# Performance work log

Measured on AMD Instinct MI355X. Metric: run time of the kernel, lower is better.

## Reference

```python
import jax, jax.numpy as jnp
import numpy as np

N_VOX = 100000   # active voxels
K = 27           # 3^3 kernel offsets
M = 60000        # matched (in, out) pairs per offset
CIN = 64
COUT = 64
BN_EPS = 1e-5


def setup_inputs() -> dict:
    key = jax.random.key(0)
    ks = jax.random.split(key, 6)
    feats = jax.random.normal(ks[0], (N_VOX, CIN), dtype=jnp.float32)
    W = jax.random.normal(ks[1], (K, CIN, COUT), dtype=jnp.float32) * 0.05
    gamma = jnp.ones((COUT,), dtype=jnp.float32)
    beta = jnp.zeros((COUT,), dtype=jnp.float32)
    running_mean = jax.random.normal(ks[2], (COUT,), dtype=jnp.float32) * 0.1
    running_var = jax.random.uniform(ks[3], (COUT,), dtype=jnp.float32, minval=0.5, maxval=1.5)
    in_idx = jax.random.randint(ks[4], (K, M), 0, N_VOX, dtype=jnp.int32)
    out_idx = jax.random.randint(ks[5], (K, M), 0, N_VOX, dtype=jnp.int32)
    return {
        "feats": feats, "W": W, "gamma": gamma, "beta": beta,
        "running_mean": running_mean, "running_var": running_var,
        "in_idx": in_idx, "out_idx": out_idx,
    }


def reference(feats, W, gamma, beta, running_mean, running_var, in_idx, out_idx):
    # Sparse conv as gather-GEMM-scatter over the hash-map kernel map.
    gathered = feats[in_idx]                              # [K, M, Cin]
    contrib = jnp.einsum('kmc,kcd->kmd', gathered, W)     # [K, M, Cout]
    out = jax.ops.segment_sum(
        contrib.reshape(-1, W.shape[-1]),                 # [K*M, Cout]
        out_idx.reshape(-1),
        num_segments=feats.shape[0],
    )                                                     # [N, Cout]
    # BatchNorm (inference, running stats) + ReLU
    inv = jax.lax.rsqrt(running_var + BN_EPS)
    y = (out - running_mean) * (inv * gamma) + beta
    return jnp.maximum(y, 0.0)
```

## Files before the change

kernel.cpp:

```cpp
#include <hip/hip_runtime.h>

#define N_VOX 100000
#define K_OFF 27
#define M_PAIR 60000
#define NPAIR (K_OFF * M_PAIR)
#define CIN 64
#define COUT 64
#define BN_EPS 1e-5f

#define VB_SHIFT 8
#define VB (1 << VB_SHIFT)
#define NB ((N_VOX + VB - 1) / VB)
#define BCAP 5120
#define PPT 16
#define PA_PAIRS (256 * PPT)
#define PA_GRID ((NPAIR + PA_PAIRS - 1) / PA_PAIRS)

#define TILES_PER_WAVE 10
#define WAVES_PER_K (M_PAIR / 16 / TILES_PER_WAVE)
#define CONV_BLOCKS_X ((WAVES_PER_K + 3) / 4)

typedef __attribute__((ext_vector_type(8))) short bf16x8;
typedef __attribute__((ext_vector_type(8))) unsigned short u16x8;
typedef __attribute__((ext_vector_type(2))) unsigned int u32x2;
typedef __attribute__((ext_vector_type(4))) float f32x4;

__device__ __forceinline__ unsigned short f32_to_bf16(float f) {
    unsigned int u = __float_as_uint(f);
    u += 0x7FFFu + ((u >> 16) & 1u);
    return (unsigned short)(u >> 16);
}
__device__ __forceinline__ float bf16_lo(unsigned int u) {
    return __uint_as_float(u << 16);
}
__device__ __forceinline__ float bf16_hi(unsigned int u) {
    return __uint_as_float(u & 0xffff0000u);
}
__device__ __forceinline__ float bf16_to_f32(unsigned short b) {
    return __uint_as_float(((unsigned int)b) << 16);
}

__global__ __launch_bounds__(256) void scatter_pairs_kernel(
    const int* __restrict__ oix,
    unsigned int* __restrict__ recs, int* __restrict__ bucketCount,
    const float* __restrict__ feats, unsigned short* __restrict__ fb,
    const float* __restrict__ W, unsigned short* __restrict__ Wt,
    const float* __restrict__ gamma, const float* __restrict__ beta,
    const float* __restrict__ rmean, const float* __restrict__ rvar,
    float* __restrict__ bnscale, float* __restrict__ bnshift)
{
    __shared__ int lhist[NB];
    __shared__ int gbase[NB];
    const int t = threadIdx.x;
    for (int i = t; i < NB; i += 256) lhist[i] = 0;
    __syncthreads();

    const int base = blockIdx.x * PA_PAIRS;
    int vsave[PPT];
    int lpos[PPT];
#pragma unroll
    for (int i = 0; i < PPT; ++i) {
        const int e = base + i * 256 + t;
        int v = -1, lp = 0;
        if (e < NPAIR) {
            v = oix[e];
            lp = atomicAdd(&lhist[v >> VB_SHIFT], 1);
        }
        vsave[i] = v;
        lpos[i] = lp;
    }
    __syncthreads();
    for (int i = t; i < NB; i += 256) {
        const int c = lhist[i];
        gbase[i] = c ? atomicAdd(&bucketCount[i], c) : 0;
    }
    __syncthreads();
#pragma unroll
    for (int i = 0; i < PPT; ++i) {
        const int v = vsave[i];
        if (v >= 0) {
            const int e = base + i * 256 + t;
            const int b = v >> VB_SHIFT;
            const int idx = gbase[b] + lpos[i];
            if (idx < BCAP)
                recs[(size_t)b * BCAP + idx] =
                    ((unsigned int)e << VB_SHIFT) | (unsigned int)(v & (VB - 1));
        }
    }

    const int gid = blockIdx.x * 256 + t;
    const int nt = PA_GRID * 256;
    for (int e4i = gid; e4i < (N_VOX * CIN) / 4; e4i += nt) {
        const int e4 = e4i * 4;
        const float4 v = *(const float4*)(feats + e4);
        ushort4 b;
        b.x = f32_to_bf16(v.x);
        b.y = f32_to_bf16(v.y);
        b.z = f32_to_bf16(v.z);
        b.w = f32_to_bf16(v.w);
        *(ushort4*)(fb + e4) = b;
    }
    for (int e = gid; e < K_OFF * CIN * COUT; e += nt) {
        const int k = e / (CIN * COUT);
        const int r = e % (CIN * COUT);
        Wt[k * CIN * COUT + (r % COUT) * CIN + (r / COUT)] = f32_to_bf16(W[e]);
    }
    if (gid < COUT) {
        const float inv = rsqrtf(rvar[gid] + BN_EPS);
        const float sc = inv * gamma[gid];
        bnscale[gid] = sc;
        bnshift[gid] = beta[gid] - rmean[gid] * sc;
    }
}

__global__ __launch_bounds__(256) void rank_kernel(
    const unsigned int* __restrict__ recs, const int* __restrict__ bucketCount,
    int* __restrict__ rank, int* __restrict__ cntc)
{
    __shared__ int hist[VB];
    const int b = blockIdx.x;
    const int t = threadIdx.x;
    hist[t] = 0;
    __syncthreads();
    int bc = bucketCount[b];
    if (bc > BCAP) bc = BCAP;
    const unsigned int* r = recs + (size_t)b * BCAP;
    for (int i = t; i < bc; i += 256) {
        const unsigned int rec = r[i];
        const int vl = rec & (VB - 1);
        const int pid = rec >> VB_SHIFT;
        rank[pid] = atomicAdd(&hist[vl], 1);
    }
    __syncthreads();
    const int v = b * VB + t;
    if (v < N_VOX) cntc[v] = hist[t];
}

__global__ __launch_bounds__(256) void alloc_kernel(
    const int* __restrict__ cntc, int* __restrict__ total, int* __restrict__ seg)
{
    __shared__ int part[256];
    __shared__ int bbase;
    const int t = threadIdx.x;
    const int v = blockIdx.x * 256 + t;
    const int c = (v < N_VOX) ? cntc[v] : 0;
    part[t] = c;
    __syncthreads();
    for (int o = 1; o < 256; o <<= 1) {
        int x = (t >= o) ? part[t - o] : 0;
        __syncthreads();
        part[t] += x;
        __syncthreads();
    }
    if (t == 255) bbase = atomicAdd(total, part[255]);
    __syncthreads();
    if (v < N_VOX) seg[v] = bbase + (part[t] - c);
}

__global__ __launch_bounds__(256) void conv_scatter_kernel(
    const unsigned short* __restrict__ fb, const unsigned short* __restrict__ Wt,
    const int* __restrict__ in_idx, const int* __restrict__ out_idx,
    const int* __restrict__ rank, const int* __restrict__ seg,
    unsigned short* __restrict__ contrib)
{
    __shared__ alignas(16) unsigned short lds[4][16 * 72];
    const int k = blockIdx.y;
    const int lane = threadIdx.x & 63;
    const int wid = threadIdx.x >> 6;
    const int w = blockIdx.x * 4 + wid;
    if (w >= WAVES_PER_K) return;
    const int col = lane & 15;
    const int quad = lane >> 4;
    unsigned short* L = lds[wid];

    bf16x8 Bf[4][2];
    const short* Wk = (const short*)(Wt + k * CIN * COUT);
#pragma unroll
    for (int t = 0; t < 4; ++t) {
        const short* p = Wk + (t * 16 + col) * CIN + quad * 8;
        Bf[t][0] = *(const bf16x8*)(p);
        Bf[t][1] = *(const bf16x8*)(p + 32);
    }

    int m0 = k * M_PAIR + (w * TILES_PER_WAVE) * 16;
    int slot = 0;
    if (lane < 16) slot = seg[out_idx[m0 + lane]] + rank[m0 + lane];
    {
        const int rin = in_idx[m0 + col];
        const short* fp = (const short*)fb + (size_t)rin * CIN + quad * 8;
        bf16x8 A0 = *(const bf16x8*)(fp);
        bf16x8 A1 = *(const bf16x8*)(fp + 32);

        for (int it = 0; it < TILES_PER_WAVE; ++it) {
            bf16x8 nA0 = A0, nA1 = A1;
            int nslot = slot;
            if (it + 1 < TILES_PER_WAVE) {
                const int m1 = m0 + 16;
                if (lane < 16)
                    nslot = seg[out_idx[m1 + lane]] + rank[m1 + lane];
                const int rn = in_idx[m1 + col];
                const short* fn = (const short*)fb + (size_t)rn * CIN + quad * 8;
                nA0 = *(const bf16x8*)(fn);
                nA1 = *(const bf16x8*)(fn + 32);
            }

            f32x4 acc[4];
#pragma unroll
            for (int t = 0; t < 4; ++t) {
                f32x4 z = {0.f, 0.f, 0.f, 0.f};
                acc[t] = __builtin_amdgcn_mfma_f32_16x16x32_bf16(A0, Bf[t][0], z, 0, 0, 0);
                acc[t] = __builtin_amdgcn_mfma_f32_16x16x32_bf16(A1, Bf[t][1], acc[t], 0, 0, 0);
            }
#pragma unroll
            for (int r = 0; r < 4; ++r) {
                const int row = quad * 4 + r;
#pragma unroll
                for (int t = 0; t < 4; ++t)
                    L[row * 72 + t * 16 + col] = f32_to_bf16(acc[t][r]);
            }
#pragma unroll
            for (int itr = 0; itr < 2; ++itr) {
                const int row = itr * 8 + (lane >> 3);
                const int chunk = lane & 7;
                const int pos = __shfl(slot, row, 64);
                const u16x8 v = *(const u16x8*)(L + row * 72 + chunk * 8);
                __builtin_nontemporal_store(
                    v, (u16x8*)(contrib + (size_t)pos * 64 + chunk * 8));
            }
            A0 = nA0;
            A1 = nA1;
            slot = nslot;
            m0 += 16;
        }
    }
}

__global__ __launch_bounds__(256) void gather_bn_kernel(
    const unsigned short* __restrict__ contrib, const int* __restrict__ seg,
    const int* __restrict__ cntc,
    const float* __restrict__ bnscale, const float* __restrict__ bnshift,
    float* __restrict__ out)
{
    const int v = blockIdx.x * 4 + (threadIdx.x >> 6);
    if (v >= N_VOX) return;
    const int lane = threadIdx.x & 63;
    const int rg = lane >> 4;
    const int cg = lane & 15;
    const int s = seg[v];
    const int n = cntc[v];

    const u32x2* base = (const u32x2*)(contrib + (size_t)s * 64) + cg;
    float a0 = 0.f, a1 = 0.f, a2 = 0.f, a3 = 0.f;
    float b0 = 0.f, b1 = 0.f, b2 = 0.f, b3 = 0.f;
    int j = rg;
    for (; j + 4 < n; j += 8) {
        const u32x2 u = __builtin_nontemporal_load(base + (size_t)j * 16);
        const u32x2 w = __builtin_nontemporal_load(base + (size_t)(j + 4) * 16);
        a0 += bf16_lo(u.x); a1 += bf16_hi(u.x);
        a2 += bf16_lo(u.y); a3 += bf16_hi(u.y);
        b0 += bf16_lo(w.x); b1 += bf16_hi(w.x);
        b2 += bf16_lo(w.y); b3 += bf16_hi(w.y);
    }
    for (; j < n; j += 4) {
        const u32x2 u = __builtin_nontemporal_load(base + (size_t)j * 16);
        a0 += bf16_lo(u.x); a1 += bf16_hi(u.x);
        a2 += bf16_lo(u.y); a3 += bf16_hi(u.y);
    }
    a0 += b0; a1 += b1; a2 += b2; a3 += b3;
    a0 += __shfl_xor(a0, 16, 64); a0 += __shfl_xor(a0, 32, 64);
    a1 += __shfl_xor(a1, 16, 64); a1 += __shfl_xor(a1, 32, 64);
    a2 += __shfl_xor(a2, 16, 64); a2 += __shfl_xor(a2, 32, 64);
    a3 += __shfl_xor(a3, 16, 64); a3 += __shfl_xor(a3, 32, 64);
    if (rg == 0) {
        const int ch = cg * 4;
        float4 r;
        r.x = fmaxf(fmaf(a0, bnscale[ch + 0], bnshift[ch + 0]), 0.f);
        r.y = fmaxf(fmaf(a1, bnscale[ch + 1], bnshift[ch + 1]), 0.f);
        r.z = fmaxf(fmaf(a2, bnscale[ch + 2], bnshift[ch + 2]), 0.f);
        r.w = fmaxf(fmaf(a3, bnscale[ch + 3], bnshift[ch + 3]), 0.f);
        *(float4*)(out + (size_t)v * 64 + ch) = r;
    }
}

__global__ __launch_bounds__(256) void prep_small_kernel(
    const float* __restrict__ feats, unsigned short* __restrict__ fb,
    float* __restrict__ out, const float* __restrict__ W,
    unsigned short* __restrict__ Wt)
{
    const int e = blockIdx.x * blockDim.x + threadIdx.x;
    if (e < (N_VOX * CIN) / 4) {
        const int e4 = e * 4;
        const float4 v = *(const float4*)(feats + e4);
        ushort4 b;
        b.x = f32_to_bf16(v.x);
        b.y = f32_to_bf16(v.y);
        b.z = f32_to_bf16(v.z);
        b.w = f32_to_bf16(v.w);
        *(ushort4*)(fb + e4) = b;
        *(float4*)(out + e4) = make_float4(0.f, 0.f, 0.f, 0.f);
    }
    if (e < K_OFF * CIN * COUT) {
        const int k = e / (CIN * COUT);
        const int r = e % (CIN * COUT);
        Wt[k * CIN * COUT + (r % COUT) * CIN + (r / COUT)] = f32_to_bf16(W[e]);
    }
}

__global__ __launch_bounds__(256) void conv_atomic_kernel(
    const unsigned short* __restrict__ fb, const unsigned short* __restrict__ Wt,
    const int* __restrict__ in_idx, const int* __restrict__ out_idx,
    float* __restrict__ out)
{
    const int k = blockIdx.y;
    const int lane = threadIdx.x & 63;
    const int wave = blockIdx.x * 4 + (threadIdx.x >> 6);
    const int col = lane & 15;
    const int quad = lane >> 4;
    bf16x8 Bf[4][2];
    const short* Wk = (const short*)(Wt + k * CIN * COUT);
#pragma unroll
    for (int t = 0; t < 4; ++t) {
        const short* p = Wk + (t * 16 + col) * CIN + quad * 8;
        Bf[t][0] = *(const bf16x8*)(p);
        Bf[t][1] = *(const bf16x8*)(p + 32);
    }
    const int base = k * M_PAIR;
    for (int tile = wave; tile < M_PAIR / 16; tile += 128) {
        const int m0 = base + tile * 16;
        const int rin = in_idx[m0 + col];
        const short* fp = (const short*)fb + (size_t)rin * CIN + quad * 8;
        const bf16x8 A0 = *(const bf16x8*)(fp);
        const bf16x8 A1 = *(const bf16x8*)(fp + 32);
        f32x4 acc[4];
#pragma unroll
        for (int t = 0; t < 4; ++t) {
            f32x4 z = {0.f, 0.f, 0.f, 0.f};
            acc[t] = __builtin_amdgcn_mfma_f32_16x16x32_bf16(A0, Bf[t][0], z, 0, 0, 0);
            acc[t] = __builtin_amdgcn_mfma_f32_16x16x32_bf16(A1, Bf[t][1], acc[t], 0, 0, 0);
        }
        int vo[4];
#pragma unroll
        for (int r = 0; r < 4; ++r) vo[r] = out_idx[m0 + quad * 4 + r];
#pragma unroll
        for (int r = 0; r < 4; ++r) {
            float* op = out + (size_t)vo[r] * COUT + col;
#pragma unroll
            for (int t = 0; t < 4; ++t) atomicAdd(op + t * 16, acc[t][r]);
        }
    }
}

__global__ __launch_bounds__(256) void bn_relu_kernel(
    float* __restrict__ out,
    const float* __restrict__ gamma, const float* __restrict__ beta,
    const float* __restrict__ mean, const float* __restrict__ var)
{
    const int e = blockIdx.x * blockDim.x + threadIdx.x;
    if (e >= N_VOX * COUT) return;
    const int c = e & (COUT - 1);
    const float inv = rsqrtf(var[c] + BN_EPS);
    const float y = (out[e] - mean[c]) * (inv * gamma[c]) + beta[c];
    out[e] = fmaxf(y, 0.f);
}

extern "C" void kernel_launch(void* const* d_in, const int* in_sizes, int n_in,
                              void* d_out, int out_size, void* d_ws, size_t ws_size,
                              hipStream_t stream) {
    const float* feats = (const float*)d_in[0];
    const float* W     = (const float*)d_in[1];
    const float* gamma = (const float*)d_in[2];
    const float* beta  = (const float*)d_in[3];
    const float* rmean = (const float*)d_in[4];
    const float* rvar  = (const float*)d_in[5];
    const int* in_idx  = (const int*)d_in[6];
    const int* out_idx = (const int*)d_in[7];
    float* out = (float*)d_out;

    char* ws = (char*)d_ws;
    size_t off = 0;
    auto alloc = [&](size_t bytes) {
        size_t p = off;
        off = (off + bytes + 255) & ~(size_t)255;
        return p;
    };
    const size_t o_fb   = alloc((size_t)N_VOX * CIN * 2);
    const size_t o_wt   = alloc((size_t)K_OFF * CIN * COUT * 2);
    const size_t o_bc   = alloc((size_t)NB * 4 + 4);
    const size_t o_recs = alloc((size_t)NB * BCAP * 4);
    const size_t o_seg  = alloc((size_t)N_VOX * 4);
    const size_t o_cntc = alloc((size_t)N_VOX * 4);
    const size_t o_bn   = alloc((size_t)2 * COUT * 4);
    const size_t o_rank = alloc((size_t)NPAIR * 4);
    const size_t o_ctr  = alloc((size_t)NPAIR * COUT * 2);
    const bool big = (ws_size >= off);

    unsigned short* fb  = (unsigned short*)(ws + o_fb);
    unsigned short* Wt  = (unsigned short*)(ws + o_wt);
    int* bucketCount    = (int*)(ws + o_bc);
    int* total          = bucketCount + NB;
    unsigned int* recs  = (unsigned int*)(ws + o_recs);
    int* seg            = (int*)(ws + o_seg);
    int* cntc           = (int*)(ws + o_cntc);
    float* bnscale      = (float*)(ws + o_bn);
    float* bnshift      = bnscale + COUT;
    int* rank           = (int*)(ws + o_rank);
    unsigned short* ctr = (unsigned short*)(ws + o_ctr);

    if (big) {
        hipError_t _e = hipMemsetAsync(bucketCount, 0, (size_t)NB * 4 + 4, stream);
        (void)_e;
        scatter_pairs_kernel<<<PA_GRID, 256, 0, stream>>>(
            out_idx, recs, bucketCount, feats, fb, W, Wt,
            gamma, beta, rmean, rvar, bnscale, bnshift);
        rank_kernel<<<NB, 256, 0, stream>>>(recs, bucketCount, rank, cntc);
        alloc_kernel<<<(N_VOX + 255) / 256, 256, 0, stream>>>(cntc, total, seg);
        conv_scatter_kernel<<<dim3(CONV_BLOCKS_X, K_OFF), 256, 0, stream>>>(
            fb, Wt, in_idx, out_idx, rank, seg, ctr);
        gather_bn_kernel<<<(N_VOX + 3) / 4, 256, 0, stream>>>(
            ctr, seg, cntc, bnscale, bnshift, out);
    } else {
        const int ptot = (N_VOX * CIN) / 4;
        prep_small_kernel<<<(ptot + 255) / 256, 256, 0, stream>>>(feats, fb, out, W, Wt);
        conv_atomic_kernel<<<dim3(32, K_OFF), 256, 0, stream>>>(fb, Wt, in_idx, out_idx, out);
        const int total_e = N_VOX * COUT;
        bn_relu_kernel<<<(total_e + 255) / 256, 256, 0, stream>>>(out, gamma, beta, rmean, rvar);
    }
}
```

Baseline: 253.7 us.

## Write conv results in pair order and gather via a per-voxel permutation

The conv kernel previously scattered each bf16 contribution row to a slot grouped by output voxel, which needed seg and rank lookups per pair. It now writes contributions contiguously in pair order. A new bucket scan plus perm_seg kernel builds a permutation list sorted by output voxel, and the gather kernel reads rows indirectly through it using 16-byte loads and 8 lanes per row. This removes index lookups and scattered writes from the conv stage but makes the gather reads random, one row per pair, with an extra perm load each.

```diff
diff --git a/kernel.cpp b/kernel.cpp
--- a/kernel.cpp
+++ b/kernel.cpp
@@ -22,7 +22,7 @@
 
 typedef __attribute__((ext_vector_type(8))) short bf16x8;
 typedef __attribute__((ext_vector_type(8))) unsigned short u16x8;
-typedef __attribute__((ext_vector_type(2))) unsigned int u32x2;
+typedef __attribute__((ext_vector_type(4))) unsigned int u32x4;
 typedef __attribute__((ext_vector_type(4))) float f32x4;
 
 __device__ __forceinline__ unsigned short f32_to_bf16(float f) {
@@ -35,9 +35,6 @@
 }
 __device__ __forceinline__ float bf16_hi(unsigned int u) {
     return __uint_as_float(u & 0xffff0000u);
-}
-__device__ __forceinline__ float bf16_to_f32(unsigned short b) {
-    return __uint_as_float(((unsigned int)b) << 16);
 }
 
 __global__ __launch_bounds__(256) void scatter_pairs_kernel(
@@ -113,11 +110,34 @@
     }
 }
 
-__global__ __launch_bounds__(256) void rank_kernel(
+__global__ __launch_bounds__(512) void bucket_scan_kernel(
+    const int* __restrict__ bucketCount, int* __restrict__ bucketBase)
+{
+    __shared__ int part[512];
+    const int t = threadIdx.x;
+    int c = 0;
+    if (t < NB) {
+        c = bucketCount[t];
+        if (c > BCAP) c = BCAP;
+    }
+    part[t] = c;
+    __syncthreads();
+    for (int o = 1; o < 512; o <<= 1) {
+        int x = (t >= o) ? part[t - o] : 0;
+        __syncthreads();
+        part[t] += x;
+        __syncthreads();
+    }
+    if (t < NB) bucketBase[t] = part[t] - c;
+}
+
+__global__ __launch_bounds__(256) void perm_seg_kernel(
     const unsigned int* __restrict__ recs, const int* __restrict__ bucketCount,
-    int* __restrict__ rank, int* __restrict__ cntc)
+    const int* __restrict__ bucketBase,
+    int* __restrict__ perm, int* __restrict__ seg, int* __restrict__ cntc)
 {
     __shared__ int hist[VB];
+    __shared__ int part[VB];
     const int b = blockIdx.x;
     const int t = threadIdx.x;
     hist[t] = 0;
@@ -125,25 +145,10 @@
     int bc = bucketCount[b];
     if (bc > BCAP) bc = BCAP;
     const unsigned int* r = recs + (size_t)b * BCAP;
-    for (int i = t; i < bc; i += 256) {
-        const unsigned int rec = r[i];
-        const int vl = rec & (VB - 1);
-        const int pid = rec >> VB_SHIFT;
-        rank[pid] = atomicAdd(&hist[vl], 1);
-    }
-    __syncthreads();
-    const int v = b * VB + t;
-    if (v < N_VOX) cntc[v] = hist[t];
-}
-
-__global__ __launch_bounds__(256) void alloc_kernel(
-    const int* __restrict__ cntc, int* __restrict__ total, int* __restrict__ seg)
-{
-    __shared__ int part[256];
-    __shared__ int bbase;
-    const int t = threadIdx.x;
-    const int v = blockIdx.x * 256 + t;
-    const int c = (v < N_VOX) ? cntc[v] : 0;
+    for (int i = t; i < bc; i += 256)
+        atomicAdd(&hist[r[i] & (VB - 1)], 1);
+    __syncthreads();
+    const int c = hist[t];
     part[t] = c;
     __syncthreads();
     for (int o = 1; o < 256; o <<= 1) {
@@ -152,15 +157,26 @@
         part[t] += x;
         __syncthreads();
     }
-    if (t == 255) bbase = atomicAdd(total, part[255]);
-    __syncthreads();
-    if (v < N_VOX) seg[v] = bbase + (part[t] - c);
-}
-
-__global__ __launch_bounds__(256) void conv_scatter_kernel(
+    const int gbase = bucketBase[b];
+    const int excl = part[t] - c;
+    const int v = b * VB + t;
+    if (v < N_VOX) {
+        seg[v] = gbase + excl;
+        cntc[v] = c;
+    }
+    __syncthreads();
+    hist[t] = excl;
+    __syncthreads();
+    for (int i = t; i < bc; i += 256) {
+        const unsigned int rec = r[i];
+        const int lp = atomicAdd(&hist[rec & (VB - 1)], 1);
+        perm[gbase + lp] = (int)(rec >> VB_SHIFT);
+    }
+}
+
+__global__ __launch_bounds__(256) void conv_kernel(
     const unsigned short* __restrict__ fb, const unsigned short* __restrict__ Wt,
-    const int* __restrict__ in_idx, const int* __restrict__ out_idx,
-    const int* __restrict__ rank, const int* __restrict__ seg,
+    const int* __restrict__ in_idx,
     unsigned short* __restrict__ contrib)
 {
     __shared__ alignas(16) unsigned short lds[4][16 * 72];
@@ -183,8 +199,6 @@
     }
 
     int m0 = k * M_PAIR + (w * TILES_PER_WAVE) * 16;
-    int slot = 0;
-    if (lane < 16) slot = seg[out_idx[m0 + lane]] + rank[m0 + lane];
     {
         const int rin = in_idx[m0 + col];
         const short* fp = (const short*)fb + (size_t)rin * CIN + quad * 8;
@@ -193,12 +207,8 @@
 
         for (int it = 0; it < TILES_PER_WAVE; ++it) {
             bf16x8 nA0 = A0, nA1 = A1;
-            int nslot = slot;
             if (it + 1 < TILES_PER_WAVE) {
-                const int m1 = m0 + 16;
-                if (lane < 16)
-                    nslot = seg[out_idx[m1 + lane]] + rank[m1 + lane];
-                const int rn = in_idx[m1 + col];
+                const int rn = in_idx[m0 + 16 + col];
                 const short* fn = (const short*)fb + (size_t)rn * CIN + quad * 8;
                 nA0 = *(const bf16x8*)(fn);
                 nA1 = *(const bf16x8*)(fn + 32);
@@ -222,63 +232,84 @@
             for (int itr = 0; itr < 2; ++itr) {
                 const int row = itr * 8 + (lane >> 3);
                 const int chunk = lane & 7;
-                const int pos = __shfl(slot, row, 64);
                 const u16x8 v = *(const u16x8*)(L + row * 72 + chunk * 8);
                 __builtin_nontemporal_store(
-                    v, (u16x8*)(contrib + (size_t)pos * 64 + chunk * 8));
+                    v, (u16x8*)(contrib + (size_t)(m0 + row) * 64 + chunk * 8));
             }
             A0 = nA0;
             A1 = nA1;
-            slot = nslot;
             m0 += 16;
         }
     }
 }
 
 __global__ __launch_bounds__(256) void gather_bn_kernel(
-    const unsigned short* __restrict__ contrib, const int* __restrict__ seg,
-    const int* __restrict__ cntc,
+    const unsigned short* __restrict__ contrib, const int* __restrict__ perm,
+    const int* __restrict__ seg, const int* __restrict__ cntc,
     const float* __restrict__ bnscale, const float* __restrict__ bnshift,
     float* __restrict__ out)
 {
     const int v = blockIdx.x * 4 + (threadIdx.x >> 6);
     if (v >= N_VOX) return;
     const int lane = threadIdx.x & 63;
-    const int rg = lane >> 4;
-    const int cg = lane & 15;
+    const int rg = lane >> 3;
+    const int cg = lane & 7;
     const int s = seg[v];
     const int n = cntc[v];
 
-    const u32x2* base = (const u32x2*)(contrib + (size_t)s * 64) + cg;
     float a0 = 0.f, a1 = 0.f, a2 = 0.f, a3 = 0.f;
+    float a4 = 0.f, a5 = 0.f, a6 = 0.f, a7 = 0.f;
     float b0 = 0.f, b1 = 0.f, b2 = 0.f, b3 = 0.f;
+    float b4 = 0.f, b5 = 0.f, b6 = 0.f, b7 = 0.f;
     int j = rg;
-    for (; j + 4 < n; j += 8) {
-        const u32x2 u = __builtin_nontemporal_load(base + (size_t)j * 16);
-        const u32x2 w = __builtin_nontemporal_load(base + (size_t)(j + 4) * 16);
+    for (; j + 8 < n; j += 16) {
+        const int p0 = perm[s + j];
+        const int p1 = perm[s + j + 8];
+        const u32x4 u = __builtin_nontemporal_load(
+            (const u32x4*)(contrib + (size_t)p0 * 64) + cg);
+        const u32x4 w = __builtin_nontemporal_load(
+            (const u32x4*)(contrib + (size_t)p1 * 64) + cg);
         a0 += bf16_lo(u.x); a1 += bf16_hi(u.x);
         a2 += bf16_lo(u.y); a3 += bf16_hi(u.y);
+        a4 += bf16_lo(u.z); a5 += bf16_hi(u.z);
+        a6 += bf16_lo(u.w); a7 += bf16_hi(u.w);
         b0 += bf16_lo(w.x); b1 += bf16_hi(w.x);
         b2 += bf16_lo(w.y); b3 += bf16_hi(w.y);
-    }
-    for (; j < n; j += 4) {
-        const u32x2 u = __builtin_nontemporal_load(base + (size_t)j * 16);
+        b4 += bf16_lo(w.z); b5 += bf16_hi(w.z);
+        b6 += bf16_lo(w.w); b7 += bf16_hi(w.w);
+    }
+    for (; j < n; j += 8) {
+        const int p0 = perm[s + j];
+        const u32x4 u = __builtin_nontemporal_load(
+            (const u32x4*)(contrib + (size_t)p0 * 64) + cg);
         a0 += bf16_lo(u.x); a1 += bf16_hi(u.x);
         a2 += bf16_lo(u.y); a3 += bf16_hi(u.y);
+        a4 += bf16_lo(u.z); a5 += bf16_hi(u.z);
+        a6 += bf16_lo(u.w); a7 += bf16_hi(u.w);
     }
     a0 += b0; a1 += b1; a2 += b2; a3 += b3;
-    a0 += __shfl_xor(a0, 16, 64); a0 += __shfl_xor(a0, 32, 64);
-    a1 += __shfl_xor(a1, 16, 64); a1 += __shfl_xor(a1, 32, 64);
-    a2 += __shfl_xor(a2, 16, 64); a2 += __shfl_xor(a2, 32, 64);
-    a3 += __shfl_xor(a3, 16, 64); a3 += __shfl_xor(a3, 32, 64);
+    a4 += b4; a5 += b5; a6 += b6; a7 += b7;
+    a0 += __shfl_xor(a0, 8, 64); a0 += __shfl_xor(a0, 16, 64); a0 += __shfl_xor(a0, 32, 64);
+    a1 += __shfl_xor(a1, 8, 64); a1 += __shfl_xor(a1, 16, 64); a1 += __shfl_xor(a1, 32, 64);
+    a2 += __shfl_xor(a2, 8, 64); a2 += __shfl_xor(a2, 16, 64); a2 += __shfl_xor(a2, 32, 64);
+    a3 += __shfl_xor(a3, 8, 64); a3 += __shfl_xor(a3, 16, 64); a3 += __shfl_xor(a3, 32, 64);
+    a4 += __shfl_xor(a4, 8, 64); a4 += __shfl_xor(a4, 16, 64); a4 += __shfl_xor(a4, 32, 64);
+    a5 += __shfl_xor(a5, 8, 64); a5 += __shfl_xor(a5, 16, 64); a5 += __shfl_xor(a5, 32, 64);
+    a6 += __shfl_xor(a6, 8, 64); a6 += __shfl_xor(a6, 16, 64); a6 += __shfl_xor(a6, 32, 64);
+    a7 += __shfl_xor(a7, 8, 64); a7 += __shfl_xor(a7, 16, 64); a7 += __shfl_xor(a7, 32, 64);
     if (rg == 0) {
-        const int ch = cg * 4;
-        float4 r;
-        r.x = fmaxf(fmaf(a0, bnscale[ch + 0], bnshift[ch + 0]), 0.f);
-        r.y = fmaxf(fmaf(a1, bnscale[ch + 1], bnshift[ch + 1]), 0.f);
-        r.z = fmaxf(fmaf(a2, bnscale[ch + 2], bnshift[ch + 2]), 0.f);
-        r.w = fmaxf(fmaf(a3, bnscale[ch + 3], bnshift[ch + 3]), 0.f);
-        *(float4*)(out + (size_t)v * 64 + ch) = r;
+        const int ch = cg * 8;
+        float4 r0, r1;
+        r0.x = fmaxf(fmaf(a0, bnscale[ch + 0], bnshift[ch + 0]), 0.f);
+        r0.y = fmaxf(fmaf(a1, bnscale[ch + 1], bnshift[ch + 1]), 0.f);
+        r0.z = fmaxf(fmaf(a2, bnscale[ch + 2], bnshift[ch + 2]), 0.f);
+        r0.w = fmaxf(fmaf(a3, bnscale[ch + 3], bnshift[ch + 3]), 0.f);
+        r1.x = fmaxf(fmaf(a4, bnscale[ch + 4], bnshift[ch + 4]), 0.f);
+        r1.y = fmaxf(fmaf(a5, bnscale[ch + 5], bnshift[ch + 5]), 0.f);
+        r1.z = fmaxf(fmaf(a6, bnscale[ch + 6], bnshift[ch + 6]), 0.f);
+        r1.w = fmaxf(fmaf(a7, bnscale[ch + 7], bnshift[ch + 7]), 0.f);
+        *(float4*)(out + (size_t)v * 64 + ch) = r0;
+        *(float4*)(out + (size_t)v * 64 + ch + 4) = r1;
     }
 }
 
@@ -385,39 +416,41 @@
     };
     const size_t o_fb   = alloc((size_t)N_VOX * CIN * 2);
     const size_t o_wt   = alloc((size_t)K_OFF * CIN * COUT * 2);
-    const size_t o_bc   = alloc((size_t)NB * 4 + 4);
+    const size_t o_bc   = alloc((size_t)NB * 4);
+    const size_t o_bb   = alloc((size_t)NB * 4);
     const size_t o_recs = alloc((size_t)NB * BCAP * 4);
     const size_t o_seg  = alloc((size_t)N_VOX * 4);
     const size_t o_cntc = alloc((size_t)N_VOX * 4);
     const size_t o_bn   = alloc((size_t)2 * COUT * 4);
-    const size_t o_rank = alloc((size_t)NPAIR * 4);
+    const size_t o_perm = alloc((size_t)NPAIR * 4);
     const size_t o_ctr  = alloc((size_t)NPAIR * COUT * 2);
     const bool big = (ws_size >= off);
 
     unsigned short* fb  = (unsigned short*)(ws + o_fb);
     unsigned short* Wt  = (unsigned short*)(ws + o_wt);
     int* bucketCount    = (int*)(ws + o_bc);
-    int* total          = bucketCount + NB;
+    int* bucketBase     = (int*)(ws + o_bb);
     unsigned int* recs  = (unsigned int*)(ws + o_recs);
     int* seg            = (int*)(ws + o_seg);
     int* cntc           = (int*)(ws + o_cntc);
     float* bnscale      = (float*)(ws + o_bn);
     float* bnshift      = bnscale + COUT;
-    int* rank           = (int*)(ws + o_rank);
+    int* perm           = (int*)(ws + o_perm);
     unsigned short* ctr = (unsigned short*)(ws + o_ctr);
 
     if (big) {
-        hipError_t _e = hipMemsetAsync(bucketCount, 0, (size_t)NB * 4 + 4, stream);
+        hipError_t _e = hipMemsetAsync(bucketCount, 0, (size_t)NB * 4, stream);
         (void)_e;
         scatter_pairs_kernel<<<PA_GRID, 256, 0, stream>>>(
             out_idx, recs, bucketCount, feats, fb, W, Wt,
             gamma, beta, rmean, rvar, bnscale, bnshift);
-        rank_kernel<<<NB, 256, 0, stream>>>(recs, bucketCount, rank, cntc);
-        alloc_kernel<<<(N_VOX + 255) / 256, 256, 0, stream>>>(cntc, total, seg);
-        conv_scatter_kernel<<<dim3(CONV_BLOCKS_X, K_OFF), 256, 0, stream>>>(
-            fb, Wt, in_idx, out_idx, rank, seg, ctr);
+        bucket_scan_kernel<<<1, 512, 0, stream>>>(bucketCount, bucketBase);
+        perm_seg_kernel<<<NB, 256, 0, stream>>>(recs, bucketCount, bucketBase,
+                                                perm, seg, cntc);
+        conv_kernel<<<dim3(CONV_BLOCKS_X, K_OFF), 256, 0, stream>>>(
+            fb, Wt, in_idx, ctr);
         gather_bn_kernel<<<(N_VOX + 3) / 4, 256, 0, stream>>>(
-            ctr, seg, cntc, bnscale, bnshift, out);
+            ctr, perm, seg, cntc, bnscale, bnshift, out);
     } else {
         const int ptot = (N_VOX * CIN) / 4;
         prep_small_kernel<<<(ptot + 255) / 256, 256, 0, stream>>>(feats, fb, out, W, Wt);
```

New measurement: 254.4 us. No clear change (+0.3%).
